# Kernel tuning notes

Measured on AMD Instinct MI355X. Metric: run time of the kernel, lower is better.

Reference implementation:

```python
import jax, jax.numpy as jnp
import numpy as np

N_NODES = 50000
N_EDGES = 625000
IN_DIM = 128
OUT_DIM = 128


def setup_inputs() -> dict:
    key = jax.random.key(0)
    ks = jax.random.split(key, 8)
    feats = jax.random.normal(ks[0], (N_NODES, IN_DIM), dtype=jnp.float32)
    src = jax.random.randint(ks[1], (N_EDGES,), 0, N_NODES, dtype=jnp.int64)
    dst = jax.random.randint(ks[2], (N_EDGES,), 0, N_NODES, dtype=jnp.int64)
    # nn.Linear default init: U(-1/sqrt(fan_in), 1/sqrt(fan_in))
    bf = 1.0 / np.sqrt(IN_DIM)
    W_f = jax.random.uniform(ks[3], (OUT_DIM, IN_DIM), jnp.float32, -bf, bf)
    b_f = jax.random.uniform(ks[4], (OUT_DIM,), jnp.float32, -bf, bf)
    bp = 1.0 / np.sqrt(OUT_DIM)
    W_phy = jax.random.uniform(ks[5], (OUT_DIM, OUT_DIM), jnp.float32, -bp, bp)
    b_phy = jax.random.uniform(ks[6], (OUT_DIM,), jnp.float32, -bp, bp)
    eps = jnp.zeros((1,), dtype=jnp.float32)  # init_eps = 0
    return {"feats": feats, "src": src, "dst": dst, "W_f": W_f, "b_f": b_f,
            "W_phy": W_phy, "b_phy": b_phy, "eps": eps}


def reference(feats, src, dst, W_f, b_f, W_phy, b_phy, eps):
    # mlp_f (num_mlps=1): linear + relu
    h = jax.nn.relu(feats @ W_f.T + b_f)              # [N, out_dim]
    # update_all(copy_u('h'), sum): sum messages h[src] at dst
    n = jax.ops.segment_sum(h[src], dst, num_segments=N_NODES)  # [N, out_dim]
    # faithful to source: h = 1 + eps * h + n
    h = 1.0 + eps * h + n
    # mlp_phy (num_mlps=1): linear + relu
    h = jax.nn.relu(h @ W_phy.T + b_phy)
    return h
```

## Files before the change

kernel.cpp:

```cpp
#include <hip/hip_runtime.h>

#define N_NODES 50000
#define N_EDGES 625000
#define DIM 128
#define CAP 64

typedef __bf16 bf16x8 __attribute__((ext_vector_type(8)));
typedef __bf16 bf16x4 __attribute__((ext_vector_type(4)));
typedef __bf16 bf16x2 __attribute__((ext_vector_type(2)));
typedef float f32x4 __attribute__((ext_vector_type(4)));

__device__ __forceinline__ float bflo(unsigned u) { return __uint_as_float(u << 16); }
__device__ __forceinline__ float bfhi(unsigned u) { return __uint_as_float(u & 0xffff0000u); }

__global__ __launch_bounds__(512) void gemm1_fill_k(
    const float* __restrict__ A_f32,
    const float* __restrict__ W,
    const float* __restrict__ bias,
    __bf16* __restrict__ out_bf16,
    const int* __restrict__ src,
    const int* __restrict__ dst,
    int* __restrict__ cnt,
    int* __restrict__ bucket,
    int gemm_blocks)
{
    const int t = threadIdx.x;

    if ((int)blockIdx.x >= gemm_blocks) {
        if ((int)blockIdx.x == gemm_blocks && t < 16) {
            bf16x8 z = {};
            *(bf16x8*)&out_bf16[(size_t)N_NODES * DIM + t * 8] = z;
        }
        int idx = ((int)blockIdx.x - gemm_blocks) * 512 + t;
        if (idx < N_EDGES / 4) {
            int4 s4 = ((const int4*)src)[idx];
            int4 d4 = ((const int4*)dst)[idx];
            int p0 = atomicAdd(&cnt[d4.x], 1);
            bucket[(d4.x << 6) + p0] = s4.x;
            int p1 = atomicAdd(&cnt[d4.y], 1);
            bucket[(d4.y << 6) + p1] = s4.y;
            int p2 = atomicAdd(&cnt[d4.z], 1);
            bucket[(d4.z << 6) + p2] = s4.z;
            int p3 = atomicAdd(&cnt[d4.w], 1);
            bucket[(d4.w << 6) + p3] = s4.w;
        }
        return;
    }

    __shared__ __align__(16) __bf16 w_lds[128 * 136];

    for (int i = t; i < 4096; i += 512) {
        float4 f = ((const float4*)W)[i];
        int n = i >> 5;
        int k = (i & 31) << 2;
        bf16x4 pk = { (__bf16)f.x, (__bf16)f.y, (__bf16)f.z, (__bf16)f.w };
        *(bf16x4*)&w_lds[n * 136 + k] = pk;
    }
    __syncthreads();

    const int wave = t >> 6;
    const int lane = t & 63;
    const int q = lane >> 4;
    const int mr = lane & 15;

    const int m0 = blockIdx.x * 128 + wave * 16;
    int arow = m0 + mr;
    if (arow >= N_NODES) arow = N_NODES - 1;

    f32x4 acc[8] = {};

#pragma unroll
    for (int ks = 0; ks < 4; ++ks) {
        const int k0 = ks * 32 + q * 8;
        const float4* ap = (const float4*)&A_f32[(size_t)arow * DIM + k0];
        float4 a0 = ap[0], a1 = ap[1];
        bf16x8 af;
        af[0] = (__bf16)a0.x; af[1] = (__bf16)a0.y;
        af[2] = (__bf16)a0.z; af[3] = (__bf16)a0.w;
        af[4] = (__bf16)a1.x; af[5] = (__bf16)a1.y;
        af[6] = (__bf16)a1.z; af[7] = (__bf16)a1.w;
#pragma unroll
        for (int nt = 0; nt < 8; ++nt) {
            bf16x8 bfr = *(const bf16x8*)&w_lds[(nt * 16 + mr) * 136 + k0];
            acc[nt] = __builtin_amdgcn_mfma_f32_16x16x32_bf16(af, bfr, acc[nt], 0, 0, 0);
        }
    }

    __syncthreads();
    float* lds_f = (float*)w_lds;
    const int nb = blockIdx.x * 128;

#pragma unroll
    for (int half = 0; half < 2; ++half) {
        if ((wave >> 2) == half) {
            int lw = wave & 3;
#pragma unroll
            for (int nt = 0; nt < 8; ++nt)
#pragma unroll
                for (int r = 0; r < 4; ++r)
                    lds_f[(lw * 16 + q * 4 + r) * 132 + nt * 16 + mr] = acc[nt][r];
        }
        __syncthreads();
        for (int i = t; i < 2048; i += 512) {
            int lr = i >> 5;
            int cg = (i & 31) << 2;
            int grow = nb + half * 64 + lr;
            if (grow < N_NODES) {
                float4 v = *(const float4*)&lds_f[lr * 132 + cg];
                float4 b4 = *(const float4*)&bias[cg];
                bf16x4 o;
                o[0] = (__bf16)fmaxf(v.x + b4.x, 0.f);
                o[1] = (__bf16)fmaxf(v.y + b4.y, 0.f);
                o[2] = (__bf16)fmaxf(v.z + b4.z, 0.f);
                o[3] = (__bf16)fmaxf(v.w + b4.w, 0.f);
                *(bf16x4*)&out_bf16[(size_t)grow * DIM + cg] = o;
            }
        }
        __syncthreads();
    }
}

__global__ __launch_bounds__(256) void agg_combine_k(
    const __bf16* __restrict__ h,
    const int* __restrict__ cnt,
    const int* __restrict__ bucket,
    const float* __restrict__ eps_p,
    __bf16* __restrict__ c)
{
    const int t = threadIdx.x;
    const int node = blockIdx.x * 4 + (t >> 6);
    const int lane = t & 63;
    const int ch = lane << 1;

    const int deg = cnt[node];
    const int base = node << 6;
    const int ZROW = N_NODES;

    float ax = 0.f, ay = 0.f;
    for (int e = 0; e < deg; e += 4) {
        uint4 i4 = *(const uint4*)&bucket[base + e];
        int s0 = (int)i4.x;
        int s1 = (e + 1 < deg) ? (int)i4.y : ZROW;
        int s2 = (e + 2 < deg) ? (int)i4.z : ZROW;
        int s3 = (e + 3 < deg) ? (int)i4.w : ZROW;
        unsigned v0 = *(const unsigned*)&h[(size_t)s0 * DIM + ch];
        unsigned v1 = *(const unsigned*)&h[(size_t)s1 * DIM + ch];
        unsigned v2 = *(const unsigned*)&h[(size_t)s2 * DIM + ch];
        unsigned v3 = *(const unsigned*)&h[(size_t)s3 * DIM + ch];
        ax += bflo(v0) + bflo(v1) + bflo(v2) + bflo(v3);
        ay += bfhi(v0) + bfhi(v1) + bfhi(v2) + bfhi(v3);
    }

    const float eps = eps_p[0];
    unsigned sv = *(const unsigned*)&h[(size_t)node * DIM + ch];
    bf16x2 o;
    o[0] = (__bf16)(1.0f + eps * bflo(sv) + ax);
    o[1] = (__bf16)(1.0f + eps * bfhi(sv) + ay);
    *(bf16x2*)&c[(size_t)node * DIM + ch] = o;
}

__global__ __launch_bounds__(512) void gemm2_k(
    const __bf16* __restrict__ A,
    const float* __restrict__ W,
    const float* __restrict__ bias,
    float* __restrict__ out)
{
    __shared__ __align__(16) __bf16 w_lds[128 * 136];

    const int t = threadIdx.x;

    for (int i = t; i < 4096; i += 512) {
        float4 f = ((const float4*)W)[i];
        int n = i >> 5;
        int k = (i & 31) << 2;
        bf16x4 pk = { (__bf16)f.x, (__bf16)f.y, (__bf16)f.z, (__bf16)f.w };
        *(bf16x4*)&w_lds[n * 136 + k] = pk;
    }
    __syncthreads();

    const int wave = t >> 6;
    const int lane = t & 63;
    const int q = lane >> 4;
    const int mr = lane & 15;

    const int m0 = blockIdx.x * 128 + wave * 16;
    int arow = m0 + mr;
    if (arow >= N_NODES) arow = N_NODES - 1;

    f32x4 acc[8] = {};

#pragma unroll
    for (int ks = 0; ks < 4; ++ks) {
        const int k0 = ks * 32 + q * 8;
        bf16x8 af = *(const bf16x8*)&A[(size_t)arow * DIM + k0];
#pragma unroll
        for (int nt = 0; nt < 8; ++nt) {
            bf16x8 bfr = *(const bf16x8*)&w_lds[(nt * 16 + mr) * 136 + k0];
            acc[nt] = __builtin_amdgcn_mfma_f32_16x16x32_bf16(af, bfr, acc[nt], 0, 0, 0);
        }
    }

    __syncthreads();
    float* lds_f = (float*)w_lds;
    const int nb = blockIdx.x * 128;

#pragma unroll
    for (int half = 0; half < 2; ++half) {
        if ((wave >> 2) == half) {
            int lw = wave & 3;
#pragma unroll
            for (int nt = 0; nt < 8; ++nt)
#pragma unroll
                for (int r = 0; r < 4; ++r)
                    lds_f[(lw * 16 + q * 4 + r) * 132 + nt * 16 + mr] = acc[nt][r];
        }
        __syncthreads();
        for (int i = t; i < 2048; i += 512) {
            int lr = i >> 5;
            int cg = (i & 31) << 2;
            int grow = nb + half * 64 + lr;
            if (grow < N_NODES) {
                float4 v = *(const float4*)&lds_f[lr * 132 + cg];
                float4 b4 = *(const float4*)&bias[cg];
                v.x = fmaxf(v.x + b4.x, 0.f);
                v.y = fmaxf(v.y + b4.y, 0.f);
                v.z = fmaxf(v.z + b4.z, 0.f);
                v.w = fmaxf(v.w + b4.w, 0.f);
                *(float4*)&out[(size_t)grow * DIM + cg] = v;
            }
        }
        __syncthreads();
    }
}

extern "C" void kernel_launch(void* const* d_in, const int* in_sizes, int n_in,
                              void* d_out, int out_size, void* d_ws, size_t ws_size,
                              hipStream_t stream) {
    const float* feats = (const float*)d_in[0];
    const int*   src   = (const int*)d_in[1];
    const int*   dst   = (const int*)d_in[2];
    const float* W_f   = (const float*)d_in[3];
    const float* b_f   = (const float*)d_in[4];
    const float* W_phy = (const float*)d_in[5];
    const float* b_phy = (const float*)d_in[6];
    const float* eps   = (const float*)d_in[7];
    float* out = (float*)d_out;

    const size_t HN = (size_t)(N_NODES + 1) * DIM;
    __bf16* h   = (__bf16*)d_ws;
    __bf16* c   = h + HN;
    int* bucket = (int*)(c + (size_t)N_NODES * DIM);
    int* cnt    = bucket + (size_t)N_NODES * CAP;

    const int gblocks = (N_NODES + 127) / 128;
    const int fblocks = (N_EDGES / 4 + 511) / 512;

    hipMemsetAsync(cnt, 0, N_NODES * sizeof(int), stream);

    gemm1_fill_k<<<gblocks + fblocks, 512, 0, stream>>>(
        feats, W_f, b_f, h, src, dst, cnt, bucket, gblocks);

    agg_combine_k<<<N_NODES / 4, 256, 0, stream>>>(
        h, cnt, bucket, eps, c);

    gemm2_k<<<gblocks, 512, 0, stream>>>(
        c, W_phy, b_phy, out);
}
```

Before: 161.2 us.

## Fuse neighbor aggregation with second GEMM via LDS-staged combined rows

Merges the aggregation/combine kernel and the second GEMM into one kernel. Each 256-thread block aggregates 64 nodes into LDS as bf16, then runs MFMA on them directly, which removes the global round trip of the intermediate matrix and one launch. W_phy is converted to bf16 once inside the first kernel, and B fragments are read from global/L2 instead of LDS. Each wave now walks 16 nodes serially, so there are fewer in-flight gathers per block and the output is written with uncoalesced scalar stores instead of an LDS-transposed float4 epilogue.

```diff
diff --git a/kernel.cpp b/kernel.cpp
--- a/kernel.cpp
+++ b/kernel.cpp
@@ -22,14 +22,23 @@
     const int* __restrict__ dst,
     int* __restrict__ cnt,
     int* __restrict__ bucket,
+    const float* __restrict__ W_phy,
+    __bf16* __restrict__ Wb,
     int gemm_blocks)
 {
     const int t = threadIdx.x;
 
     if ((int)blockIdx.x >= gemm_blocks) {
-        if ((int)blockIdx.x == gemm_blocks && t < 16) {
-            bf16x8 z = {};
-            *(bf16x8*)&out_bf16[(size_t)N_NODES * DIM + t * 8] = z;
+        if ((int)blockIdx.x == gemm_blocks) {
+            if (t < 16) {
+                bf16x8 z = {};
+                *(bf16x8*)&out_bf16[(size_t)N_NODES * DIM + t * 8] = z;
+            }
+            for (int i = t; i < 4096; i += 512) {
+                float4 f = ((const float4*)W_phy)[i];
+                bf16x4 pk = { (__bf16)f.x, (__bf16)f.y, (__bf16)f.z, (__bf16)f.w };
+                *(bf16x4*)&Wb[i * 4] = pk;
+            }
         }
         int idx = ((int)blockIdx.x - gemm_blocks) * 512 + t;
         if (idx < N_EDGES / 4) {
@@ -120,116 +129,78 @@
     }
 }
 
-__global__ __launch_bounds__(256) void agg_combine_k(
+__global__ __launch_bounds__(256) void agg_gemm2_k(
     const __bf16* __restrict__ h,
     const int* __restrict__ cnt,
     const int* __restrict__ bucket,
     const float* __restrict__ eps_p,
-    __bf16* __restrict__ c)
-{
-    const int t = threadIdx.x;
-    const int node = blockIdx.x * 4 + (t >> 6);
-    const int lane = t & 63;
-    const int ch = lane << 1;
-
-    const int deg = cnt[node];
-    const int base = node << 6;
-    const int ZROW = N_NODES;
-
-    float ax = 0.f, ay = 0.f;
-    for (int e = 0; e < deg; e += 4) {
-        uint4 i4 = *(const uint4*)&bucket[base + e];
-        int s0 = (int)i4.x;
-        int s1 = (e + 1 < deg) ? (int)i4.y : ZROW;
-        int s2 = (e + 2 < deg) ? (int)i4.z : ZROW;
-        int s3 = (e + 3 < deg) ? (int)i4.w : ZROW;
-        unsigned v0 = *(const unsigned*)&h[(size_t)s0 * DIM + ch];
-        unsigned v1 = *(const unsigned*)&h[(size_t)s1 * DIM + ch];
-        unsigned v2 = *(const unsigned*)&h[(size_t)s2 * DIM + ch];
-        unsigned v3 = *(const unsigned*)&h[(size_t)s3 * DIM + ch];
-        ax += bflo(v0) + bflo(v1) + bflo(v2) + bflo(v3);
-        ay += bfhi(v0) + bfhi(v1) + bfhi(v2) + bfhi(v3);
-    }
-
-    const float eps = eps_p[0];
-    unsigned sv = *(const unsigned*)&h[(size_t)node * DIM + ch];
-    bf16x2 o;
-    o[0] = (__bf16)(1.0f + eps * bflo(sv) + ax);
-    o[1] = (__bf16)(1.0f + eps * bfhi(sv) + ay);
-    *(bf16x2*)&c[(size_t)node * DIM + ch] = o;
-}
-
-__global__ __launch_bounds__(512) void gemm2_k(
-    const __bf16* __restrict__ A,
-    const float* __restrict__ W,
+    const __bf16* __restrict__ Wb,
     const float* __restrict__ bias,
     float* __restrict__ out)
 {
-    __shared__ __align__(16) __bf16 w_lds[128 * 136];
+    __shared__ __align__(16) __bf16 c_lds[64 * 136];
 
     const int t = threadIdx.x;
-
-    for (int i = t; i < 4096; i += 512) {
-        float4 f = ((const float4*)W)[i];
-        int n = i >> 5;
-        int k = (i & 31) << 2;
-        bf16x4 pk = { (__bf16)f.x, (__bf16)f.y, (__bf16)f.z, (__bf16)f.w };
-        *(bf16x4*)&w_lds[n * 136 + k] = pk;
-    }
-    __syncthreads();
-
     const int wave = t >> 6;
     const int lane = t & 63;
+    const int ch = lane << 1;
+    const int nb = blockIdx.x * 64;
+    const int ZROW = N_NODES;
+    const float eps = eps_p[0];
+
+    for (int i = 0; i < 16; ++i) {
+        int node = nb + wave * 16 + i;
+        if (node >= N_NODES) node = N_NODES - 1;
+        const int deg = cnt[node];
+        const int base = node << 6;
+
+        float ax = 0.f, ay = 0.f;
+        for (int e = 0; e < deg; e += 4) {
+            uint4 i4 = *(const uint4*)&bucket[base + e];
+            int s0 = (int)i4.x;
+            int s1 = (e + 1 < deg) ? (int)i4.y : ZROW;
+            int s2 = (e + 2 < deg) ? (int)i4.z : ZROW;
+            int s3 = (e + 3 < deg) ? (int)i4.w : ZROW;
+            unsigned v0 = *(const unsigned*)&h[(size_t)s0 * DIM + ch];
+            unsigned v1 = *(const unsigned*)&h[(size_t)s1 * DIM + ch];
+            unsigned v2 = *(const unsigned*)&h[(size_t)s2 * DIM + ch];
+            unsigned v3 = *(const unsigned*)&h[(size_t)s3 * DIM + ch];
+            ax += bflo(v0) + bflo(v1) + bflo(v2) + bflo(v3);
+            ay += bfhi(v0) + bfhi(v1) + bfhi(v2) + bfhi(v3);
+        }
+        unsigned sv = *(const unsigned*)&h[(size_t)node * DIM + ch];
+        bf16x2 o;
+        o[0] = (__bf16)(1.0f + eps * bflo(sv) + ax);
+        o[1] = (__bf16)(1.0f + eps * bfhi(sv) + ay);
+        *(bf16x2*)&c_lds[(wave * 16 + i) * 136 + ch] = o;
+    }
+    __syncthreads();
+
     const int q = lane >> 4;
     const int mr = lane & 15;
 
-    const int m0 = blockIdx.x * 128 + wave * 16;
-    int arow = m0 + mr;
-    if (arow >= N_NODES) arow = N_NODES - 1;
-
     f32x4 acc[8] = {};
-
 #pragma unroll
     for (int ks = 0; ks < 4; ++ks) {
         const int k0 = ks * 32 + q * 8;
-        bf16x8 af = *(const bf16x8*)&A[(size_t)arow * DIM + k0];
+        bf16x8 af = *(const bf16x8*)&c_lds[(wave * 16 + mr) * 136 + k0];
 #pragma unroll
         for (int nt = 0; nt < 8; ++nt) {
-            bf16x8 bfr = *(const bf16x8*)&w_lds[(nt * 16 + mr) * 136 + k0];
+            bf16x8 bfr = *(const bf16x8*)&Wb[(nt * 16 + mr) * DIM + k0];
             acc[nt] = __builtin_amdgcn_mfma_f32_16x16x32_bf16(af, bfr, acc[nt], 0, 0, 0);
         }
     }
 
-    __syncthreads();
-    float* lds_f = (float*)w_lds;
-    const int nb = blockIdx.x * 128;
-
-#pragma unroll
-    for (int half = 0; half < 2; ++half) {
-        if ((wave >> 2) == half) {
-            int lw = wave & 3;
-#pragma unroll
-            for (int nt = 0; nt < 8; ++nt)
-#pragma unroll
-                for (int r = 0; r < 4; ++r)
-                    lds_f[(lw * 16 + q * 4 + r) * 132 + nt * 16 + mr] = acc[nt][r];
-        }
-        __syncthreads();
-        for (int i = t; i < 2048; i += 512) {
-            int lr = i >> 5;
-            int cg = (i & 31) << 2;
-            int grow = nb + half * 64 + lr;
-            if (grow < N_NODES) {
-                float4 v = *(const float4*)&lds_f[lr * 132 + cg];
-                float4 b4 = *(const float4*)&bias[cg];
-                v.x = fmaxf(v.x + b4.x, 0.f);
-                v.y = fmaxf(v.y + b4.y, 0.f);
-                v.z = fmaxf(v.z + b4.z, 0.f);
-                v.w = fmaxf(v.w + b4.w, 0.f);
-                *(float4*)&out[(size_t)grow * DIM + cg] = v;
-            }
-        }
-        __syncthreads();
+    const int m0 = nb + wave * 16;
+#pragma unroll
+    for (int nt = 0; nt < 8; ++nt) {
+        float b = bias[nt * 16 + mr];
+#pragma unroll
+        for (int r = 0; r < 4; ++r) {
+            int grow = m0 + q * 4 + r;
+            if (grow < N_NODES)
+                out[(size_t)grow * DIM + nt * 16 + mr] = fmaxf(acc[nt][r] + b, 0.f);
+        }
     }
 }
 
@@ -248,21 +219,19 @@
 
     const size_t HN = (size_t)(N_NODES + 1) * DIM;
     __bf16* h   = (__bf16*)d_ws;
-    __bf16* c   = h + HN;
-    int* bucket = (int*)(c + (size_t)N_NODES * DIM);
+    int* bucket = (int*)(h + HN);
     int* cnt    = bucket + (size_t)N_NODES * CAP;
+    __bf16* Wb  = (__bf16*)(cnt + N_NODES);
 
     const int gblocks = (N_NODES + 127) / 128;
     const int fblocks = (N_EDGES / 4 + 511) / 512;
+    const int ablocks = (N_NODES + 63) / 64;
 
     hipMemsetAsync(cnt, 0, N_NODES * sizeof(int), stream);
 
     gemm1_fill_k<<<gblocks + fblocks, 512, 0, stream>>>(
-        feats, W_f, b_f, h, src, dst, cnt, bucket, gblocks);
-
-    agg_combine_k<<<N_NODES / 4, 256, 0, stream>>>(
-        h, cnt, bucket, eps, c);
-
-    gemm2_k<<<gblocks, 512, 0, stream>>>(
-        c, W_phy, b_phy, out);
+        feats, W_f, b_f, h, src, dst, cnt, bucket, W_phy, Wb, gblocks);
+
+    agg_gemm2_k<<<ablocks, 256, 0, stream>>>(
+        h, cnt, bucket, eps, Wb, b_phy, out);
 }
```

New measurement: 190.1 us. 17.9% more time.
